# Performance work log

Hardware: AMD Instinct MI355X
Metric: run time of the kernel (lower is better)

## Reference

```python
import math
import jax, jax.numpy as jnp
import numpy as np

N, S, E, H = 8, 1024, 768, 12  # batch, seq_len, n_embed, n_head


def setup_inputs() -> dict:
    key = jax.random.key(0)
    ks = jax.random.split(key, 10)
    s = 1.0 / math.sqrt(E)
    x = jax.random.normal(ks[0], (N, S, E), dtype=jnp.float32)
    # per-head full-width projections, stacked over heads: [H, E, E] (Linear weight layout [out, in])
    Wq = jax.random.normal(ks[1], (H, E, E), dtype=jnp.float32) * s
    Wk = jax.random.normal(ks[2], (H, E, E), dtype=jnp.float32) * s
    Wv = jax.random.normal(ks[3], (H, E, E), dtype=jnp.float32) * s
    bq = jax.random.normal(ks[4], (H, E), dtype=jnp.float32) * s
    bk = jax.random.normal(ks[5], (H, E), dtype=jnp.float32) * s
    bv = jax.random.normal(ks[6], (H, E), dtype=jnp.float32) * s
    Wc = jax.random.normal(ks[7], (E, H * E), dtype=jnp.float32) * (1.0 / math.sqrt(H * E))
    bc = jax.random.normal(ks[8], (E,), dtype=jnp.float32) * s
    return {"x": x, "Wq": Wq, "bq": bq, "Wk": Wk, "bk": bk, "Wv": Wv, "bv": bv, "Wc": Wc, "bc": bc}


def reference(x, Wq, bq, Wk, bk, Wv, bv, Wc, bc):
    # Full-width QKV per head: [H, N, S, E]
    q = jnp.einsum('nse,hde->hnsd', x, Wq) + bq[:, None, None, :]
    k = jnp.einsum('nse,hde->hnsd', x, Wk) + bk[:, None, None, :]
    v = jnp.einsum('nse,hde->hnsd', x, Wv) + bv[:, None, None, :]
    # scores scaled by sqrt(n_embed) (source quirk: full n_embed, not head_dim)
    scores = jnp.einsum('hnsd,hntd->hnst', q, k) / math.sqrt(E)
    causal = jnp.tril(jnp.ones((S, S), dtype=bool))
    scores = jnp.where(causal[None, None, :, :], scores, -jnp.inf)
    # dropout applied before softmax in source; p=0 (eval) -> identity
    attn = jax.nn.softmax(scores, axis=-1)
    heads = jnp.einsum('hnst,hntd->hnsd', attn, v)  # [H, N, S, E]
    concat = jnp.transpose(heads, (1, 2, 0, 3)).reshape(N, S, H * E)
    return concat @ Wc.T + bc
```

## Files before the change

kernel.cpp:

```cpp
#include <hip/hip_runtime.h>
#include <hip/hip_bf16.h>
#include <stdint.h>

#define SEQ    1024
#define NBAT   8
#define EMB    768
#define NHEAD  12
#define MROWS  (NBAT*SEQ)
#define SCALE_S 0.03608439182435161f

typedef unsigned short u16;
typedef __attribute__((ext_vector_type(8))) short bf16x8;
typedef __attribute__((ext_vector_type(4))) float f32x4;

typedef void __attribute__((address_space(1)))* gas_ptr;
typedef void __attribute__((address_space(3)))* las_ptr;

__device__ __forceinline__ void gload16(const void* g, void* l) {
  __builtin_amdgcn_global_load_lds((gas_ptr)(void*)g, (las_ptr)l, 16, 0, 0);
}

#define VMCNT0 asm volatile("s_waitcnt vmcnt(0)" ::: "memory")
#define VMCNT2 asm volatile("s_waitcnt vmcnt(2)" ::: "memory")
#define VMCNT4 asm volatile("s_waitcnt vmcnt(4)" ::: "memory")
#define LGKM0  asm volatile("s_waitcnt lgkmcnt(0)" ::: "memory")
#define BARRIER asm volatile("s_barrier" ::: "memory")

__device__ __forceinline__ u16 f2bf(float f) {
  union { float f; uint32_t u; } a; a.f = f;
  uint32_t r = a.u + 0x7fffu + ((a.u >> 16) & 1u);
  return (u16)(r >> 16);
}
__device__ __forceinline__ uint32_t pack2(float a, float b) {
  return (uint32_t)f2bf(a) | ((uint32_t)f2bf(b) << 16);
}

__global__ void k_cvt(const float* __restrict__ s, u16* __restrict__ d, long n) {
  long i = ((long)blockIdx.x*blockDim.x + threadIdx.x)*8;
  if (i >= n) return;
  float4 a = *(const float4*)(s+i);
  float4 b = *(const float4*)(s+i+4);
  uint4 o; o.x = pack2(a.x,a.y); o.y = pack2(a.z,a.w);
  o.z = pack2(b.x,b.y); o.w = pack2(b.z,b.w);
  *(uint4*)(d+i) = o;
}

__global__ void k_cvt3(const float* __restrict__ s0, const float* __restrict__ s1,
                       const float* __restrict__ s2, u16* __restrict__ d0,
                       u16* __restrict__ d1, u16* __restrict__ d2, long n) {
  const float* s = blockIdx.z == 0 ? s0 : (blockIdx.z == 1 ? s1 : s2);
  u16* d = blockIdx.z == 0 ? d0 : (blockIdx.z == 1 ? d1 : d2);
  long i = ((long)blockIdx.x*blockDim.x + threadIdx.x)*8;
  if (i >= n) return;
  float4 a = *(const float4*)(s+i);
  float4 b = *(const float4*)(s+i+4);
  uint4 o; o.x = pack2(a.x,a.y); o.y = pack2(a.z,a.w);
  o.z = pack2(b.x,b.y); o.w = pack2(b.z,b.w);
  *(uint4*)(d+i) = o;
}

__global__ void k_cvtwc(const float* __restrict__ wc, u16* __restrict__ d, int Gi, int h0) {
  long ncol = (long)Gi*EMB;
  long i = ((long)blockIdx.x*blockDim.x + threadIdx.x)*4;
  if (i >= 768*ncol) return;
  long eo = i / ncol, c = i - eo*ncol;
  long g = c / EMB, dd = c - g*EMB;
  const float* s = wc + eo*(long)(NHEAD*EMB) + (h0+g)*EMB + dd;
  float4 a = *(const float4*)s;
  uint2 o; o.x = pack2(a.x,a.y); o.y = pack2(a.z,a.w);
  *(uint2*)(d+i) = o;
}

__global__ __launch_bounds__(512, 2) void k_gemm256(
    const u16* __restrict__ A, int lda,
    const u16* __restrict__ B, int ldb, int K,
    u16* __restrict__ Cb, long c_hs, int ldc,
    const float* __restrict__ bias, const float* __restrict__ bias2,
    int gsplit, int mode)
{
  __shared__ u16 lsA[2*16384];
  __shared__ u16 lsB[2*16384];

  int m0 = blockIdx.x * 256;
  int n0 = blockIdx.y * 256;
  int tid = threadIdx.x;
  int w = tid >> 6, l = tid & 63;
  int wr = w >> 2, wc = w & 3;

  const u16* gA = A + (size_t)(m0 + 32*w + (l>>3))*lda + (((l&7) ^ (l>>3)) << 3);
  const u16* gB = B + (size_t)(n0 + 32*w + (l>>3))*ldb + (((l&7) ^ (l>>3)) << 3);

#define STAGE256(t, buf) do { \
    int k0_ = (t)*64; \
    _Pragma("unroll") \
    for (int c_ = 0; c_ < 4; ++c_) \
      gload16(gA + (size_t)(c_*8)*lda + k0_, lsA + (buf)*16384 + (32*w + 8*c_)*64); \
    _Pragma("unroll") \
    for (int c_ = 0; c_ < 4; ++c_) \
      gload16(gB + (size_t)(c_*8)*ldb + k0_, lsB + (buf)*16384 + (32*w + 8*c_)*64); \
  } while(0)

  f32x4 acc[8][4];
  #pragma unroll
  for (int i = 0; i < 8; ++i)
    #pragma unroll
    for (int j = 0; j < 4; ++j) acc[i][j] = (f32x4)0.0f;

  int nt = K >> 6;
  STAGE256(0, 0);
  for (int t = 0; t < nt; ++t) {
    VMCNT0; BARRIER;
    if (t + 1 < nt) STAGE256(t+1, (t+1)&1);
    const u16* la = lsA + (t&1)*16384;
    const u16* lb = lsB + (t&1)*16384;
    #pragma unroll
    for (int ks = 0; ks < 2; ++ks) {
      int off = (((4*ks + (l>>4)) ^ (l&7)) << 3);
      bf16x8 af[8], bf_[4];
      #pragma unroll
      for (int fi = 0; fi < 8; ++fi)
        af[fi] = *(const bf16x8*)(la + (wr*128 + fi*16 + (l&15))*64 + off);
      #pragma unroll
      for (int fj = 0; fj < 4; ++fj)
        bf_[fj] = *(const bf16x8*)(lb + (wc*64 + fj*16 + (l&15))*64 + off);
      __builtin_amdgcn_s_setprio(1);
      #pragma unroll
      for (int fi = 0; fi < 8; ++fi)
        #pragma unroll
        for (int fj = 0; fj < 4; ++fj)
          acc[fi][fj] = __builtin_amdgcn_mfma_f32_16x16x32_bf16(af[fi], bf_[fj], acc[fi][fj], 0, 0, 0);
      __builtin_amdgcn_s_setprio(0);
    }
  }
#undef STAGE256

  if (mode == 0) {
    int s = n0 / 768;
    int dbase = n0 - s*768 + wc*64;
    const float* bsl = (s < gsplit) ? bias + (size_t)s*768 : bias2 + (size_t)(s - gsplit)*768;
    u16* Cs = Cb + (size_t)s*c_hs;
    #pragma unroll
    for (int fj = 0; fj < 4; ++fj) {
      int dcol = dbase + fj*16 + (l&15);
      float bb = bsl[dcol];
      #pragma unroll
      for (int fi = 0; fi < 8; ++fi) {
        #pragma unroll
        for (int r = 0; r < 4; ++r) {
          int row = m0 + wr*128 + fi*16 + (l>>4)*4 + r;
          Cs[(size_t)row*768 + dcol] = f2bf(acc[fi][fj][r] + bb);
        }
      }
    }
  } else {
    #pragma unroll
    for (int fi = 0; fi < 8; ++fi) {
      #pragma unroll
      for (int r = 0; r < 4; ++r) {
        int row = m0 + wr*128 + fi*16 + (l>>4)*4 + r;
        float bb = bias[row];
        #pragma unroll
        for (int fj = 0; fj < 4; ++fj) {
          int cbn = n0 + wc*64 + fj*16 + (l&15);
          Cb[(size_t)row*ldc + cbn] = f2bf(acc[fi][fj][r] + bb);
        }
      }
    }
  }
}

__global__ __launch_bounds__(256) void k_gemm(
    const u16* __restrict__ A, long a_hs, int lda,
    const u16* __restrict__ B, long b_hs, int ldb, int K,
    u16* Cb, float* Cf, long c_hs, int ldc,
    const float* __restrict__ bias, const float* __restrict__ bias2,
    long bias_hs, int gsplit, int mode, int swapxy)
{
  __shared__ u16 lsA[3*4096];
  __shared__ u16 lsB[3*4096];
  int g = blockIdx.z;
  const u16* Ag = A + (long)g*a_hs;
  const u16* Bg = B + (long)g*b_hs;
  int tm = swapxy ? blockIdx.y : blockIdx.x;
  int tn = swapxy ? blockIdx.x : blockIdx.y;
  int m0 = tm*128, n0 = tn*128;
  int tid = threadIdx.x;
  int w = tid >> 6, l = tid & 63;

  int srow = l >> 2;
  int scol = ((l & 3) ^ ((l >> 3) & 3)) * 8;
  const u16* ga0 = Ag + (long)(m0 + (2*w)*16   + srow)*lda + scol;
  const u16* ga1 = Ag + (long)(m0 + (2*w+1)*16 + srow)*lda + scol;
  const u16* gb0 = Bg + (long)(n0 + (2*w)*16   + srow)*ldb + scol;
  const u16* gb1 = Bg + (long)(n0 + (2*w+1)*16 + srow)*ldb + scol;

#define GSTAGE(k0, buf) do { \
// ... 48 lines not shown
#undef GSTAGE

  u16* Cbg = Cb ? Cb + (long)g*c_hs : (u16*)0;
  const float* bsel = (g < gsplit) ? bias : bias2;
  long gi = (g < gsplit) ? g : g - gsplit;
  const float* bs = bsel ? bsel + gi*bias_hs : (const float*)0;
  int rl = (l >> 4)*4, cl = l & 15;
  #pragma unroll
  for (int i = 0; i < 4; ++i) {
    #pragma unroll
    for (int j = 0; j < 4; ++j) {
      int rb = m0 + wr*64 + i*16 + rl;
      int cb = n0 + wc_*64 + j*16 + cl;
      float cbv = 0.f;
      if ((mode == 0 || mode == 2) && bs) cbv = bs[cb];
      #pragma unroll
      for (int r = 0; r < 4; ++r) {
        int rr = rb + r;
        float v = acc[i][j][r];
        v += (mode == 1) ? bs[rr] : cbv;
        size_t idx = (size_t)rr*(size_t)ldc + cb;
        if (mode <= 1) Cbg[idx] = f2bf(v);
        else if (mode == 2) Cf[idx] = v;
        else Cf[idx] += v;
      }
    }
  }
}

__global__ __launch_bounds__(512, 2) void k_attn(
    const u16* __restrict__ qb, const u16* __restrict__ kb,
    const u16* __restrict__ vtb, u16* __restrict__ hb, int ldh)
{
  __shared__ u16 kls[3*8192];
  __shared__ u16 vls[3*8192];
  __shared__ float s_t[64*68];
  __shared__ u16 p_t[64*64];
  __shared__ float e_s[64];

  int b = blockIdx.x;
  int xcd = b & 7, kk_ = b >> 3;
  int gn = xcd + 8*(kk_ >> 3), pair = kk_ & 7;
  int g = gn >> 3, n = gn & 7;

  const u16* Q  = qb  + (size_t)g*MROWS*EMB + (size_t)n*SEQ*EMB;
  const u16* Kp = kb  + (size_t)g*MROWS*EMB + (size_t)n*SEQ*EMB;
  const u16* Vt = vtb + (size_t)g*EMB*MROWS + (size_t)n*SEQ;
  u16* H = hb + (size_t)(n*SEQ)*ldh + (size_t)g*EMB;

  int tid = threadIdx.x;
  int w = tid >> 6, l = tid & 63;
  int qg = w >> 1;
  int cg = w & 1;
  int frow = l & 15;
  int fsw = frow & 7;
  int srow = tid >> 3;
  int sphys = tid & 7;
  int scol = ((sphys ^ (srow & 7)) << 3);

#define KSTAGE(base, pc, buf) do { \
    gload16((base) + (pc)*128,      kls + (buf)*8192 + w*512); \
    gload16((base) + (pc)*128 + 64, kls + (buf)*8192 + 4096 + w*512); \
  } while(0)
#define VSTAGE(vc, buf) do { \
    gload16(Vs + (size_t)((vc)*128)*MROWS,      vls + (buf)*8192 + w*512); \
    gload16(Vs + (size_t)((vc)*128 + 64)*MROWS, vls + (buf)*8192 + 4096 + w*512); \
  } while(0)

  for (int half = 0; half < 2; ++half) {
    int qt = half ? 15 - pair : pair;
    int q0 = qt * 64;
    int nt = qt + 1;

    f32x4 acc[6][4];
    #pragma unroll
    for (int i = 0; i < 6; ++i)
      #pragma unroll
      for (int j = 0; j < 4; ++j) acc[i][j] = (f32x4)0.0f;
    float m_reg = -1e30f, l_reg = 0.f;

    const u16* Qs = Q + (size_t)(q0 + srow)*EMB + scol;
    bf16x8 qreg[12][2];
    KSTAGE(Qs, 0, 0);
    KSTAGE(Qs, 1, 1);
    VMCNT2; BARRIER;
    #pragma unroll
    for (int pc = 0; pc < 6; ++pc) {
      if (pc < 4) KSTAGE(Qs, pc+2, (pc+2)%3);
      const u16* qb_ = kls + (pc%3)*8192;
      #pragma unroll
      for (int kk2 = 0; kk2 < 2; ++kk2)
        #pragma unroll
        for (int kkl = 0; kkl < 2; ++kkl)
          qreg[2*pc + kk2][kkl] = *(const bf16x8*)(qb_ + kk2*4096 + (qg*16 + frow)*64
                                                   + (((kkl*4 + (l>>4)) ^ fsw) << 3));
      if (pc < 4) { VMCNT2; } else if (pc == 4) { VMCNT0; }
      LGKM0; BARRIER;
    }

    for (int tt = 0; tt < nt; ++tt) {
      int t0 = tt*64;
      const u16* Ks = Kp + (size_t)(t0 + srow)*EMB + scol;
      const u16* Vs = Vt + (size_t)srow*MROWS + t0 + scol;
      if (tt == 0) { KSTAGE(Ks, 0, 0); KSTAGE(Ks, 1, 1); }
      VMCNT2; BARRIER;

      f32x4 sacc[2]; sacc[0] = (f32x4)0.0f; sacc[1] = (f32x4)0.0f;
      #pragma unroll
      for (int c = 0; c < 6; ++c) {
        if (c < 4)       KSTAGE(Ks, c+2, (c+2)%3);
        else if (c == 4) VSTAGE(0, 0);
        else             VSTAGE(1, 1);
        const u16* kb_ = kls + (c%3)*8192;
        __builtin_amdgcn_s_setprio(1);
        #pragma unroll
        for (int kk2 = 0; kk2 < 2; ++kk2) {
          #pragma unroll
          for (int kkl = 0; kkl < 2; ++kkl) {
            int so = ((kkl*4 + (l>>4)) ^ fsw) << 3;
            bf16x8 aq = qreg[2*c + kk2][kkl];
            #pragma unroll
            for (int cc = 0; cc < 2; ++cc) {
              bf16x8 bk_ = *(const bf16x8*)(kb_ + kk2*4096 + ((cg*2 + cc)*16 + frow)*64 + so);
              sacc[cc] = __builtin_amdgcn_mfma_f32_16x16x32_bf16(aq, bk_, sacc[cc], 0, 0, 0);
            }
          }
        }
        __builtin_amdgcn_s_setprio(0);
        if (c < 5) { VMCNT2; LGKM0; BARRIER; }
      }

      #pragma unroll
      for (int cc = 0; cc < 2; ++cc)
        #pragma unroll
        for (int r = 0; r < 4; ++r)
          s_t[(qg*16 + (l>>4)*4 + r)*68 + cg*32 + cc*16 + (l&15)] = sacc[cc][r]*SCALE_S;
      LGKM0; BARRIER;
      {
        int qglob = q0 + srow;
        int cbase = t0 + sphys*8;
        float v[8]; float mx = -1e30f;
        #pragma unroll
        for (int j = 0; j < 8; ++j) {
          float s = s_t[srow*68 + sphys*8 + j];
          if (cbase + j > qglob) s = -1e30f;
          v[j] = s; mx = fmaxf(mx, s);
        }
        mx = fmaxf(mx, __shfl_xor(mx, 1));
        mx = fmaxf(mx, __shfl_xor(mx, 2));
        mx = fmaxf(mx, __shfl_xor(mx, 4));
        float mn = fmaxf(m_reg, mx);
        float esc = __expf(m_reg - mn);
        float ps = 0.f; u16 pk[8];
        #pragma unroll
        for (int j = 0; j < 8; ++j) { float p = __expf(v[j] - mn); ps += p; pk[j] = f2bf(p); }
        ps += __shfl_xor(ps, 1); ps += __shfl_xor(ps, 2); ps += __shfl_xor(ps, 4);
        l_reg = l_reg*esc + ps; m_reg = mn;
        if (sphys == 0) e_s[srow] = esc;
        uint4 pv;
        pv.x = (uint32_t)pk[0] | ((uint32_t)pk[1] << 16);
        pv.y = (uint32_t)pk[2] | ((uint32_t)pk[3] << 16);
        pv.z = (uint32_t)pk[4] | ((uint32_t)pk[5] << 16);
        pv.w = (uint32_t)pk[6] | ((uint32_t)pk[7] << 16);
        *(uint4*)(p_t + srow*64 + ((sphys ^ (srow & 7)) << 3)) = pv;
      }
      VMCNT2; LGKM0; BARRIER;
      float er[4];
      #pragma unroll
      for (int r = 0; r < 4; ++r) er[r] = e_s[qg*16 + (l>>4)*4 + r];
      #pragma unroll
      for (int i = 0; i < 6; ++i)
        #pragma unroll
        for (int j = 0; j < 4; ++j)
          #pragma unroll
          for (int r = 0; r < 4; ++r) acc[i][j][r] *= er[r];
      bf16x8 pa[2];
      #pragma unroll
      for (int kk = 0; kk < 2; ++kk)
        pa[kk] = *(const bf16x8*)(p_t + (qg*16 + frow)*64 + (((kk*4 + (l>>4)) ^ fsw) << 3));
      bool stage_next = (tt + 1 < nt);
      const u16* Ks2 = Kp + (size_t)(t0 + 64 + srow)*EMB + scol;
      #pragma unroll
      for (int c = 0; c < 6; ++c) {
        if (c < 4)            VSTAGE(c+2, (c+2)%3);
        else if (stage_next)  { if (c == 4) KSTAGE(Ks2, 0, 0); else KSTAGE(Ks2, 1, 1); }
        const u16* vb_ = vls + (c%3)*8192;
        __builtin_amdgcn_s_setprio(1);
        #pragma unroll
        for (int cf = 0; cf < 4; ++cf) {
          #pragma unroll
          for (int kk = 0; kk < 2; ++kk) {
            bf16x8 vbf = *(const bf16x8*)(vb_ + (cg*64 + cf*16 + frow)*64 + (((kk*4 + (l>>4)) ^ fsw) << 3));
            acc[c][cf] = __builtin_amdgcn_mfma_f32_16x16x32_bf16(pa[kk], vbf, acc[c][cf], 0, 0, 0);
          }
        }
        __builtin_amdgcn_s_setprio(0);
        if (c < 4)      { VMCNT2; LGKM0; BARRIER; }
        else if (c == 4){ if (stage_next) { VMCNT2; } else { VMCNT0; } LGKM0; BARRIER; }
      }
    }
    if (sphys == 0) e_s[srow] = l_reg;
    LGKM0; BARRIER;
    float linv[4];
    #pragma unroll
    for (int r = 0; r < 4; ++r) linv[r] = 1.0f / e_s[qg*16 + (l>>4)*4 + r];
    #pragma unroll
    for (int i = 0; i < 6; ++i)
      #pragma unroll
      for (int j = 0; j < 4; ++j) {
        int col = i*128 + cg*64 + j*16 + (l & 15);
        #pragma unroll
        for (int r = 0; r < 4; ++r) {
          int row = q0 + qg*16 + (l>>4)*4 + r;
          H[(size_t)row*ldh + col] = f2bf(acc[i][j][r]*linv[r]);
        }
      }
    BARRIER;
  }
#undef KSTAGE
#undef VSTAGE
}

extern "C" void kernel_launch(void* const* d_in, const int* in_sizes, int n_in,
                              void* d_out, int out_size, void* d_ws, size_t ws_size,
                              hipStream_t stream) {
  const float* x  = (const float*)d_in[0];
  const float* Wq = (const float*)d_in[1];
  const float* bq = (const float*)d_in[2];
  const float* Wk = (const float*)d_in[3];
  const float* bk = (const float*)d_in[4];
  const float* Wv = (const float*)d_in[5];
  const float* bv = (const float*)d_in[6];
  const float* Wc = (const float*)d_in[7];
  const float* bc = (const float*)d_in[8];
  float* out = (float*)d_out;

  const size_t XB  = (size_t)MROWS*EMB*sizeof(u16);
  const size_t WHB = (size_t)EMB*EMB*sizeof(u16);
  const size_t per_g = 4*WHB + 4*XB;
  long long avail = (long long)ws_size - (long long)XB - 4096;
  int G = (int)(avail / (long long)per_g);
  if (G < 1) G = 1;
  if (G > NHEAD) G = NHEAD;

  char* ws = (char*)d_ws;
  u16* xb  = (u16*)ws;  ws += XB;
  u16* wqb = (u16*)ws;  ws += (size_t)(2*G)*WHB;
  u16* wvb = (u16*)ws;  ws += (size_t)G*WHB;
  u16* wcb = (u16*)ws;  ws += (size_t)G*WHB;
  u16* qb  = (u16*)ws;  ws += (size_t)(2*G)*XB;
  u16* vtb = (u16*)ws;  ws += (size_t)G*XB;
  u16* hbf = (u16*)ws;  ws += (size_t)G*XB;

  k_cvt<<<dim3(3072), dim3(256), 0, stream>>>(x, xb, (long)MROWS*EMB);

  for (int h0 = 0; h0 < NHEAD; h0 += G) {
    int Gi = (G < NHEAD - h0) ? G : (NHEAD - h0);
    long nw = (long)Gi*EMB*EMB;
    k_cvt3<<<dim3((unsigned)(nw/8/256), 1, 3), dim3(256), 0, stream>>>(
        Wq + (size_t)h0*EMB*EMB, Wk + (size_t)h0*EMB*EMB, Wv + (size_t)h0*EMB*EMB,
        wqb, wqb + (size_t)Gi*EMB*EMB, wvb, nw);
    k_cvtwc<<<dim3((unsigned)((768L*Gi*EMB/4)/256)), dim3(256), 0, stream>>>(Wc, wcb, Gi, h0);
    k_gemm256<<<dim3(32, 6*Gi), dim3(512), 0, stream>>>(
        xb, EMB, wqb, EMB, EMB,
        qb, (long)MROWS*EMB, 768,
        bq + (size_t)h0*EMB, bk + (size_t)h0*EMB, Gi, 0);
    k_gemm256<<<dim3(3*Gi, 32), dim3(512), 0, stream>>>(
        wvb, EMB, xb, EMB, EMB,
        vtb, 0L, MROWS,
        bv + (size_t)h0*EMB, (const float*)0, 9999, 1);
    k_attn<<<dim3(8*NBAT*Gi), dim3(512), 0, stream>>>(
        qb, qb + (size_t)Gi*MROWS*EMB, vtb, hbf, Gi*EMB);
    k_gemm<<<dim3(64, 6, 1), dim3(256), 0, stream>>>(
        hbf, 0L, Gi*EMB, wcb, 0L, Gi*EMB, Gi*EMB,
        (u16*)0, out, 0L, EMB,
        (h0 == 0 ? bc : (const float*)0), (const float*)0, 0L, 9999,
        (h0 == 0 ? 2 : 3), 0);
  }
}
```

Baseline: 1.144 ms.

## Restructure attention kernel with transposed MFMA tiles, register softmax, larger stages

Rewrites the attention kernel so scores are computed as K·Q^T with each wave owning a 32-key by 16-query slice. Softmax now runs directly on MFMA accumulator registers, using cross-wave max/sum exchange through small shared arrays instead of a full score tile in LDS. K/V staging moves to a unified 3-buffer pool with 256-wide chunks, fewer stage steps and barriers per tile, and a wider XOR swizzle. The output is written as packed 4-element bf16 stores. This adds more register pressure (24 Q fragments, 8 P fragments) and relies on new vmcnt accounting that could be fragile.

```diff
diff --git a/kernel.cpp b/kernel.cpp
--- a/kernel.cpp
+++ b/kernel.cpp
@@ -23,6 +23,7 @@
 #define VMCNT0 asm volatile("s_waitcnt vmcnt(0)" ::: "memory")
 #define VMCNT2 asm volatile("s_waitcnt vmcnt(2)" ::: "memory")
 #define VMCNT4 asm volatile("s_waitcnt vmcnt(4)" ::: "memory")
+#define VMCNT8 asm volatile("s_waitcnt vmcnt(8)" ::: "memory")
 #define LGKM0  asm volatile("s_waitcnt lgkmcnt(0)" ::: "memory")
 #define BARRIER asm volatile("s_barrier" ::: "memory")
 
@@ -276,11 +277,12 @@
     const u16* __restrict__ qb, const u16* __restrict__ kb,
     const u16* __restrict__ vtb, u16* __restrict__ hb, int ldh)
 {
-  __shared__ u16 kls[3*8192];
-  __shared__ u16 vls[3*8192];
-  __shared__ float s_t[64*68];
+  __shared__ u16 pool[3*16384];
   __shared__ u16 p_t[64*64];
-  __shared__ float e_s[64];
+  __shared__ float st_mx[128];
+  __shared__ float st_sm[128];
+  __shared__ float e_sc[64];
+  __shared__ float e_li[64];
 
   int b = blockIdx.x;
   int xcd = b & 7, kk_ = b >> 3;
@@ -294,27 +296,57 @@
 
   int tid = threadIdx.x;
   int w = tid >> 6, l = tid & 63;
-  int qg = w >> 1;
-  int cg = w & 1;
-  int frow = l & 15;
-  int fsw = frow & 7;
-  int srow = tid >> 3;
-  int sphys = tid & 7;
-  int scol = ((sphys ^ (srow & 7)) << 3);
-
-#define KSTAGE(base, pc, buf) do { \
-    gload16((base) + (pc)*128,      kls + (buf)*8192 + w*512); \
-    gload16((base) + (pc)*128 + 64, kls + (buf)*8192 + 4096 + w*512); \
+  int lo = l & 15, hi = l >> 4;
+  int khalf = w >> 2;
+  int qbase = (w & 3) * 16;
+  int myq = qbase + lo;
+  int kv0 = khalf*32 + lo;
+  int kv1 = kv0 + 16;
+
+#define KSTAGE(base, ch, buf) do { \
+    _Pragma("unroll") for (int i_ = 0; i_ < 4; ++i_) { \
+      int u_ = tid + 512*i_; \
+      gload16((base) + (size_t)(u_>>5)*EMB + ((ch)*256 + (((u_&31) ^ ((u_>>5)&31))<<3)), \
+              pool + (buf)*16384 + ((w*64 + 512*i_)<<3)); \
+    } } while(0)
+#define VSTAGE(t0v, ch, buf) do { \
+    _Pragma("unroll") for (int i_ = 0; i_ < 4; ++i_) { \
+      int u_ = tid + 512*i_; \
+      gload16(Vt + (size_t)((ch)*256 + (u_>>3))*MROWS + (t0v) + (((u_&7) ^ ((u_>>3)&7))<<3), \
+              pool + (buf)*16384 + ((w*64 + 512*i_)<<3)); \
+    } } while(0)
+
+#define QK_COMPUTE(ch) do { \
+    const u16* kb_ = pool + (ch)*16384; \
+    __builtin_amdgcn_s_setprio(1); \
+    _Pragma("unroll") for (int ks = 0; ks < 8; ++ks) { \
+      bf16x8 k0_ = *(const bf16x8*)(kb_ + ((kv0*32 + ((ks*4 + hi) ^ (kv0 & 31)))<<3)); \
+      bf16x8 k1_ = *(const bf16x8*)(kb_ + ((kv1*32 + ((ks*4 + hi) ^ (kv1 & 31)))<<3)); \
+      sacc0 = __builtin_amdgcn_mfma_f32_16x16x32_bf16(k0_, qreg[(ch)*8+ks], sacc0, 0, 0, 0); \
+      sacc1 = __builtin_amdgcn_mfma_f32_16x16x32_bf16(k1_, qreg[(ch)*8+ks], sacc1, 0, 0, 0); \
+    } \
+    __builtin_amdgcn_s_setprio(0); \
   } while(0)
-#define VSTAGE(vc, buf) do { \
-    gload16(Vs + (size_t)((vc)*128)*MROWS,      vls + (buf)*8192 + w*512); \
-    gload16(Vs + (size_t)((vc)*128 + 64)*MROWS, vls + (buf)*8192 + 4096 + w*512); \
+
+#define PV_COMPUTE(ch) do { \
+    const u16* vb_ = pool + (ch)*16384; \
+    __builtin_amdgcn_s_setprio(1); \
+    _Pragma("unroll") for (int jp = 0; jp < 2; ++jp) { \
+      int el_ = (w + 8*jp)*16 + lo; \
+      _Pragma("unroll") for (int ks2 = 0; ks2 < 2; ++ks2) { \
+        bf16x8 vf_ = *(const bf16x8*)(vb_ + (((el_<<3) + ((ks2*4 + hi) ^ (el_ & 7)))<<3)); \
+        _Pragma("unroll") for (int qf = 0; qf < 4; ++qf) \
+          acc[2*(ch)+jp][qf] = __builtin_amdgcn_mfma_f32_16x16x32_bf16(vf_, pf[ks2][qf], acc[2*(ch)+jp][qf], 0, 0, 0); \
+      } \
+    } \
+    __builtin_amdgcn_s_setprio(0); \
   } while(0)
 
   for (int half = 0; half < 2; ++half) {
     int qt = half ? 15 - pair : pair;
     int q0 = qt * 64;
     int nt = qt + 1;
+    int qabs = q0 + myq;
 
     f32x4 acc[6][4];
     #pragma unroll
@@ -323,146 +355,135 @@
       for (int j = 0; j < 4; ++j) acc[i][j] = (f32x4)0.0f;
     float m_reg = -1e30f, l_reg = 0.f;
 
-    const u16* Qs = Q + (size_t)(q0 + srow)*EMB + scol;
-    bf16x8 qreg[12][2];
-    KSTAGE(Qs, 0, 0);
-    KSTAGE(Qs, 1, 1);
-    VMCNT2; BARRIER;
-    #pragma unroll
-    for (int pc = 0; pc < 6; ++pc) {
-      if (pc < 4) KSTAGE(Qs, pc+2, (pc+2)%3);
-      const u16* qb_ = kls + (pc%3)*8192;
-      #pragma unroll
-      for (int kk2 = 0; kk2 < 2; ++kk2)
-        #pragma unroll
-        for (int kkl = 0; kkl < 2; ++kkl)
-          qreg[2*pc + kk2][kkl] = *(const bf16x8*)(qb_ + kk2*4096 + (qg*16 + frow)*64
-                                                   + (((kkl*4 + (l>>4)) ^ fsw) << 3));
-      if (pc < 4) { VMCNT2; } else if (pc == 4) { VMCNT0; }
-      LGKM0; BARRIER;
-    }
+    const u16* Qb = Q + (size_t)q0*EMB;
+    VMCNT0;
+    KSTAGE(Qb, 0, 0);
+    KSTAGE(Qb, 1, 1);
+    KSTAGE(Qb, 2, 2);
+    VMCNT8; BARRIER;
+    bf16x8 qreg[24];
+    #pragma unroll
+    for (int ks = 0; ks < 8; ++ks)
+      qreg[ks] = *(const bf16x8*)(pool + ((myq*32 + ((ks*4 + hi) ^ (myq & 31)))<<3));
+    VMCNT4; LGKM0; BARRIER;
+    KSTAGE(Kp, 0, 0);
+    #pragma unroll
+    for (int ks = 0; ks < 8; ++ks)
+      qreg[8+ks] = *(const bf16x8*)(pool + 16384 + ((myq*32 + ((ks*4 + hi) ^ (myq & 31)))<<3));
+    VMCNT4; LGKM0; BARRIER;
+    KSTAGE(Kp, 1, 1);
+    #pragma unroll
+    for (int ks = 0; ks < 8; ++ks)
+      qreg[16+ks] = *(const bf16x8*)(pool + 2*16384 + ((myq*32 + ((ks*4 + hi) ^ (myq & 31)))<<3));
+    VMCNT4; LGKM0; BARRIER;
 
     for (int tt = 0; tt < nt; ++tt) {
       int t0 = tt*64;
-      const u16* Ks = Kp + (size_t)(t0 + srow)*EMB + scol;
-      const u16* Vs = Vt + (size_t)srow*MROWS + t0 + scol;
-      if (tt == 0) { KSTAGE(Ks, 0, 0); KSTAGE(Ks, 1, 1); }
-      VMCNT2; BARRIER;
-
-      f32x4 sacc[2]; sacc[0] = (f32x4)0.0f; sacc[1] = (f32x4)0.0f;
-      #pragma unroll
-      for (int c = 0; c < 6; ++c) {
-        if (c < 4)       KSTAGE(Ks, c+2, (c+2)%3);
-        else if (c == 4) VSTAGE(0, 0);
-        else             VSTAGE(1, 1);
-        const u16* kb_ = kls + (c%3)*8192;
-        __builtin_amdgcn_s_setprio(1);
+      int nt0 = (tt + 1 < nt) ? (tt+1)*64 : 0;
+      f32x4 sacc0 = (f32x4)0.0f, sacc1 = (f32x4)0.0f;
+
+      KSTAGE(Kp + (size_t)t0*EMB, 2, 2);
+      QK_COMPUTE(0);
+      VMCNT4; LGKM0; BARRIER;
+      VSTAGE(t0, 0, 0);
+      QK_COMPUTE(1);
+      VMCNT4; LGKM0; BARRIER;
+      VSTAGE(t0, 1, 1);
+      QK_COMPUTE(2);
+      VMCNT4; LGKM0; BARRIER;
+
+      VSTAGE(t0, 2, 2);
+      float pm = -1e30f;
+      {
+        int kvb = t0 + khalf*32 + hi*4;
         #pragma unroll
-        for (int kk2 = 0; kk2 < 2; ++kk2) {
-          #pragma unroll
-          for (int kkl = 0; kkl < 2; ++kkl) {
-            int so = ((kkl*4 + (l>>4)) ^ fsw) << 3;
-            bf16x8 aq = qreg[2*c + kk2][kkl];
-            #pragma unroll
-            for (int cc = 0; cc < 2; ++cc) {
-              bf16x8 bk_ = *(const bf16x8*)(kb_ + kk2*4096 + ((cg*2 + cc)*16 + frow)*64 + so);
-              sacc[cc] = __builtin_amdgcn_mfma_f32_16x16x32_bf16(aq, bk_, sacc[cc], 0, 0, 0);
-            }
-          }
+        for (int r = 0; r < 4; ++r) {
+          float x0 = sacc0[r]*SCALE_S;
+          float x1 = sacc1[r]*SCALE_S;
+          if (kvb + r > qabs)      x0 = -1e30f;
+          if (kvb + 16 + r > qabs) x1 = -1e30f;
+          sacc0[r] = x0; sacc1[r] = x1;
+          pm = fmaxf(pm, fmaxf(x0, x1));
         }
-        __builtin_amdgcn_s_setprio(0);
-        if (c < 5) { VMCNT2; LGKM0; BARRIER; }
       }
-
-      #pragma unroll
-      for (int cc = 0; cc < 2; ++cc)
+      pm = fmaxf(pm, __shfl_xor(pm, 16));
+      pm = fmaxf(pm, __shfl_xor(pm, 32));
+      if (l < 16) st_mx[khalf*64 + myq] = pm;
+      LGKM0; BARRIER;
+      float mn = fmaxf(m_reg, fmaxf(st_mx[myq], st_mx[64 + myq]));
+      float esc = __expf(m_reg - mn);
+      m_reg = mn;
+      float p0_ = __expf(sacc0[0]-mn), p1_ = __expf(sacc0[1]-mn);
+      float p2_ = __expf(sacc0[2]-mn), p3_ = __expf(sacc0[3]-mn);
+      float p4_ = __expf(sacc1[0]-mn), p5_ = __expf(sacc1[1]-mn);
+      float p6_ = __expf(sacc1[2]-mn), p7_ = __expf(sacc1[3]-mn);
+      float ps = ((p0_+p1_)+(p2_+p3_)) + ((p4_+p5_)+(p6_+p7_));
+      ps += __shfl_xor(ps, 16);
+      ps += __shfl_xor(ps, 32);
+      if (l < 16) { st_sm[khalf*64 + myq] = ps; if (khalf == 0) e_sc[myq] = esc; }
+      {
+        int sl0 = khalf*4 + (hi>>1);
+        int ph0 = sl0 ^ (myq & 7);
+        int ph1 = (sl0 + 2) ^ (myq & 7);
+        uint2 v0; v0.x = pack2(p0_, p1_); v0.y = pack2(p2_, p3_);
+        uint2 v1; v1.x = pack2(p4_, p5_); v1.y = pack2(p6_, p7_);
+        *(uint2*)(p_t + myq*64 + ph0*8 + (hi&1)*4) = v0;
+        *(uint2*)(p_t + myq*64 + ph1*8 + (hi&1)*4) = v1;
+      }
+      LGKM0; BARRIER;
+      l_reg = l_reg*esc + st_sm[myq] + st_sm[64 + myq];
+
+      bf16x8 pf[2][4];
+      #pragma unroll
+      for (int ks2 = 0; ks2 < 2; ++ks2)
         #pragma unroll
-        for (int r = 0; r < 4; ++r)
-          s_t[(qg*16 + (l>>4)*4 + r)*68 + cg*32 + cc*16 + (l&15)] = sacc[cc][r]*SCALE_S;
-      LGKM0; BARRIER;
-      {
-        int qglob = q0 + srow;
-        int cbase = t0 + sphys*8;
-        float v[8]; float mx = -1e30f;
-        #pragma unroll
-        for (int j = 0; j < 8; ++j) {
-          float s = s_t[srow*68 + sphys*8 + j];
-          if (cbase + j > qglob) s = -1e30f;
-          v[j] = s; mx = fmaxf(mx, s);
+        for (int qf = 0; qf < 4; ++qf) {
+          int qr = qf*16 + lo;
+          pf[ks2][qf] = *(const bf16x8*)(p_t + ((qr*8 + ((ks2*4 + hi) ^ (qr & 7)))<<3));
         }
-        mx = fmaxf(mx, __shfl_xor(mx, 1));
-        mx = fmaxf(mx, __shfl_xor(mx, 2));
-        mx = fmaxf(mx, __shfl_xor(mx, 4));
-        float mn = fmaxf(m_reg, mx);
-        float esc = __expf(m_reg - mn);
-        float ps = 0.f; u16 pk[8];
-        #pragma unroll
-        for (int j = 0; j < 8; ++j) { float p = __expf(v[j] - mn); ps += p; pk[j] = f2bf(p); }
-        ps += __shfl_xor(ps, 1); ps += __shfl_xor(ps, 2); ps += __shfl_xor(ps, 4);
-        l_reg = l_reg*esc + ps; m_reg = mn;
-        if (sphys == 0) e_s[srow] = esc;
-        uint4 pv;
-        pv.x = (uint32_t)pk[0] | ((uint32_t)pk[1] << 16);
-        pv.y = (uint32_t)pk[2] | ((uint32_t)pk[3] << 16);
-        pv.z = (uint32_t)pk[4] | ((uint32_t)pk[5] << 16);
-        pv.w = (uint32_t)pk[6] | ((uint32_t)pk[7] << 16);
-        *(uint4*)(p_t + srow*64 + ((sphys ^ (srow & 7)) << 3)) = pv;
-      }
-      VMCNT2; LGKM0; BARRIER;
-      float er[4];
-      #pragma unroll
-      for (int r = 0; r < 4; ++r) er[r] = e_s[qg*16 + (l>>4)*4 + r];
+      float escq[4];
+      #pragma unroll
+      for (int qf = 0; qf < 4; ++qf) escq[qf] = e_sc[qf*16 + lo];
       #pragma unroll
       for (int i = 0; i < 6; ++i)
         #pragma unroll
-        for (int j = 0; j < 4; ++j)
+        for (int qf = 0; qf < 4; ++qf)
           #pragma unroll
-          for (int r = 0; r < 4; ++r) acc[i][j][r] *= er[r];
-      bf16x8 pa[2];
-      #pragma unroll
-      for (int kk = 0; kk < 2; ++kk)
-        pa[kk] = *(const bf16x8*)(p_t + (qg*16 + frow)*64 + (((kk*4 + (l>>4)) ^ fsw) << 3));
-      bool stage_next = (tt + 1 < nt);
-      const u16* Ks2 = Kp + (size_t)(t0 + 64 + srow)*EMB + scol;
-      #pragma unroll
-      for (int c = 0; c < 6; ++c) {
-        if (c < 4)            VSTAGE(c+2, (c+2)%3);
-        else if (stage_next)  { if (c == 4) KSTAGE(Ks2, 0, 0); else KSTAGE(Ks2, 1, 1); }
-        const u16* vb_ = vls + (c%3)*8192;
-        __builtin_amdgcn_s_setprio(1);
-        #pragma unroll
-        for (int cf = 0; cf < 4; ++cf) {
-          #pragma unroll
-          for (int kk = 0; kk < 2; ++kk) {
-            bf16x8 vbf = *(const bf16x8*)(vb_ + (cg*64 + cf*16 + frow)*64 + (((kk*4 + (l>>4)) ^ fsw) << 3));
-            acc[c][cf] = __builtin_amdgcn_mfma_f32_16x16x32_bf16(pa[kk], vbf, acc[c][cf], 0, 0, 0);
-          }
-        }
-        __builtin_amdgcn_s_setprio(0);
-        if (c < 4)      { VMCNT2; LGKM0; BARRIER; }
-        else if (c == 4){ if (stage_next) { VMCNT2; } else { VMCNT0; } LGKM0; BARRIER; }
+          for (int r = 0; r < 4; ++r) acc[i][qf][r] *= escq[qf];
+
+      PV_COMPUTE(0);
+      VMCNT4; LGKM0; BARRIER;
+      KSTAGE(Kp + (size_t)nt0*EMB, 0, 0);
+      PV_COMPUTE(1);
+      VMCNT4; LGKM0; BARRIER;
+      KSTAGE(Kp + (size_t)nt0*EMB, 1, 1);
+      PV_COMPUTE(2);
+      VMCNT4; LGKM0; BARRIER;
+    }
+
+    if (l < 16 && khalf == 0) e_li[myq] = 1.0f / l_reg;
+    LGKM0; BARRIER;
+    float li[4];
+    #pragma unroll
+    for (int qf = 0; qf < 4; ++qf) li[qf] = e_li[qf*16 + lo];
+    #pragma unroll
+    for (int j = 0; j < 6; ++j) {
+      int e_g = (j>>1)*256 + (w + 8*(j&1))*16 + hi*4;
+      #pragma unroll
+      for (int qf = 0; qf < 4; ++qf) {
+        int q_abs2 = q0 + qf*16 + lo;
+        uint2 v;
+        v.x = pack2(acc[j][qf][0]*li[qf], acc[j][qf][1]*li[qf]);
+        v.y = pack2(acc[j][qf][2]*li[qf], acc[j][qf][3]*li[qf]);
+        *(uint2*)(H + (size_t)q_abs2*ldh + e_g) = v;
       }
     }
-    if (sphys == 0) e_s[srow] = l_reg;
-    LGKM0; BARRIER;
-    float linv[4];
-    #pragma unroll
-    for (int r = 0; r < 4; ++r) linv[r] = 1.0f / e_s[qg*16 + (l>>4)*4 + r];
-    #pragma unroll
-    for (int i = 0; i < 6; ++i)
-      #pragma unroll
-      for (int j = 0; j < 4; ++j) {
-        int col = i*128 + cg*64 + j*16 + (l & 15);
-        #pragma unroll
-        for (int r = 0; r < 4; ++r) {
-          int row = q0 + qg*16 + (l>>4)*4 + r;
-          H[(size_t)row*ldh + col] = f2bf(acc[i][j][r]*linv[r]);
-        }
-      }
     BARRIER;
   }
 #undef KSTAGE
 #undef VSTAGE
+#undef QK_COMPUTE
+#undef PV_COMPUTE
 }
 
 extern "C" void kernel_launch(void* const* d_in, const int* in_sizes, int n_in,
```

Result: slower. 2.112 ms (+84.5%).

## Shrink QKV GEMM tile to 256x128 and add triple-buffered LDS prefetch

Applied to the files above, without the earlier changes.

The 256-wide GEMM now computes 256x128 output tiles, with 8 waves laid out 4x2 and each wave holding a 64x64 accumulator. LDS goes from double to triple buffering with two stages prefetched ahead, and the wait becomes a partial vmcnt(6) so the next tile's loads can stay in flight during compute. Smaller accumulators cut register pressure and double the number of blocks launched, at the cost of more redundant loads of A per output and lower MFMA reuse per LDS read.

```diff
diff --git a/kernel.cpp b/kernel.cpp
--- a/kernel.cpp
+++ b/kernel.cpp
@@ -23,6 +23,7 @@
 #define VMCNT0 asm volatile("s_waitcnt vmcnt(0)" ::: "memory")
 #define VMCNT2 asm volatile("s_waitcnt vmcnt(2)" ::: "memory")
 #define VMCNT4 asm volatile("s_waitcnt vmcnt(4)" ::: "memory")
+#define VMCNT6 asm volatile("s_waitcnt vmcnt(6)" ::: "memory")
 #define LGKM0  asm volatile("s_waitcnt lgkmcnt(0)" ::: "memory")
 #define BARRIER asm volatile("s_barrier" ::: "memory")
 
@@ -78,17 +79,18 @@
     const float* __restrict__ bias, const float* __restrict__ bias2,
     int gsplit, int mode)
 {
-  __shared__ u16 lsA[2*16384];
-  __shared__ u16 lsB[2*16384];
+  __shared__ u16 lsA[3*16384];
+  __shared__ u16 lsB[3*8192];
 
   int m0 = blockIdx.x * 256;
-  int n0 = blockIdx.y * 256;
+  int n0 = blockIdx.y * 128;
   int tid = threadIdx.x;
   int w = tid >> 6, l = tid & 63;
-  int wr = w >> 2, wc = w & 3;
+  int wr = w >> 1, wc = w & 1;
+  int lo = l & 15, hi = l >> 4;
 
   const u16* gA = A + (size_t)(m0 + 32*w + (l>>3))*lda + (((l&7) ^ (l>>3)) << 3);
-  const u16* gB = B + (size_t)(n0 + 32*w + (l>>3))*ldb + (((l&7) ^ (l>>3)) << 3);
+  const u16* gB = B + (size_t)(n0 + 16*w + (l>>3))*ldb + (((l&7) ^ (l>>3)) << 3);
 
 #define STAGE256(t, buf) do { \
     int k0_ = (t)*64; \
@@ -96,36 +98,45 @@
     for (int c_ = 0; c_ < 4; ++c_) \
       gload16(gA + (size_t)(c_*8)*lda + k0_, lsA + (buf)*16384 + (32*w + 8*c_)*64); \
     _Pragma("unroll") \
-    for (int c_ = 0; c_ < 4; ++c_) \
-      gload16(gB + (size_t)(c_*8)*ldb + k0_, lsB + (buf)*16384 + (32*w + 8*c_)*64); \
+    for (int c_ = 0; c_ < 2; ++c_) \
+      gload16(gB + (size_t)(c_*8)*ldb + k0_, lsB + (buf)*8192 + (16*w + 8*c_)*64); \
   } while(0)
 
-  f32x4 acc[8][4];
+  f32x4 acc[4][4];
   #pragma unroll
-  for (int i = 0; i < 8; ++i)
+  for (int i = 0; i < 4; ++i)
     #pragma unroll
     for (int j = 0; j < 4; ++j) acc[i][j] = (f32x4)0.0f;
 
   int nt = K >> 6;
   STAGE256(0, 0);
+  STAGE256(1, 1);
   for (int t = 0; t < nt; ++t) {
-    VMCNT0; BARRIER;
-    if (t + 1 < nt) STAGE256(t+1, (t+1)&1);
-    const u16* la = lsA + (t&1)*16384;
-    const u16* lb = lsB + (t&1)*16384;
+    if (t + 1 < nt) { VMCNT6; } else { VMCNT0; }
+    BARRIER;
+    if (t + 2 < nt) {
+      int nb = t + 2; nb -= (nb/3)*3;
+      STAGE256(t+2, nb);
+    }
+    int cb = t - (t/3)*3;
+    const u16* la = lsA + cb*16384;
+    const u16* lb = lsB + cb*8192;
     #pragma unroll
     for (int ks = 0; ks < 2; ++ks) {
-      int off = (((4*ks + (l>>4)) ^ (l&7)) << 3);
-      bf16x8 af[8], bf_[4];
-      #pragma unroll
-      for (int fi = 0; fi < 8; ++fi)
-        af[fi] = *(const bf16x8*)(la + (wr*128 + fi*16 + (l&15))*64 + off);
-      #pragma unroll
-      for (int fj = 0; fj < 4; ++fj)
-        bf_[fj] = *(const bf16x8*)(lb + (wc*64 + fj*16 + (l&15))*64 + off);
+      bf16x8 af[4], bf_[4];
+      #pragma unroll
+      for (int fi = 0; fi < 4; ++fi) {
+        int row = wr*64 + fi*16 + lo;
+        af[fi] = *(const bf16x8*)(la + row*64 + (((4*ks + hi) ^ (row & 7)) << 3));
+      }
+      #pragma unroll
+      for (int fj = 0; fj < 4; ++fj) {
+        int row = wc*64 + fj*16 + lo;
+        bf_[fj] = *(const bf16x8*)(lb + row*64 + (((4*ks + hi) ^ (row & 7)) << 3));
+      }
       __builtin_amdgcn_s_setprio(1);
       #pragma unroll
-      for (int fi = 0; fi < 8; ++fi)
+      for (int fi = 0; fi < 4; ++fi)
         #pragma unroll
         for (int fj = 0; fj < 4; ++fj)
           acc[fi][fj] = __builtin_amdgcn_mfma_f32_16x16x32_bf16(af[fi], bf_[fj], acc[fi][fj], 0, 0, 0);
@@ -141,27 +152,27 @@
     u16* Cs = Cb + (size_t)s*c_hs;
     #pragma unroll
     for (int fj = 0; fj < 4; ++fj) {
-      int dcol = dbase + fj*16 + (l&15);
+      int dcol = dbase + fj*16 + lo;
       float bb = bsl[dcol];
       #pragma unroll
-      for (int fi = 0; fi < 8; ++fi) {
+      for (int fi = 0; fi < 4; ++fi) {
         #pragma unroll
         for (int r = 0; r < 4; ++r) {
-          int row = m0 + wr*128 + fi*16 + (l>>4)*4 + r;
+          int row = m0 + wr*64 + fi*16 + hi*4 + r;
           Cs[(size_t)row*768 + dcol] = f2bf(acc[fi][fj][r] + bb);
         }
       }
     }
   } else {
     #pragma unroll
-    for (int fi = 0; fi < 8; ++fi) {
+    for (int fi = 0; fi < 4; ++fi) {
       #pragma unroll
       for (int r = 0; r < 4; ++r) {
-        int row = m0 + wr*128 + fi*16 + (l>>4)*4 + r;
+        int row = m0 + wr*64 + fi*16 + hi*4 + r;
         float bb = bias[row];
         #pragma unroll
         for (int fj = 0; fj < 4; ++fj) {
-          int cbn = n0 + wc*64 + fj*16 + (l&15);
+          int cbn = n0 + wc*64 + fj*16 + lo;
           Cb[(size_t)row*ldc + cbn] = f2bf(acc[fi][fj][r] + bb);
         }
       }
@@ -505,11 +516,11 @@
         Wq + (size_t)h0*EMB*EMB, Wk + (size_t)h0*EMB*EMB, Wv + (size_t)h0*EMB*EMB,
         wqb, wqb + (size_t)Gi*EMB*EMB, wvb, nw);
     k_cvtwc<<<dim3((unsigned)((768L*Gi*EMB/4)/256)), dim3(256), 0, stream>>>(Wc, wcb, Gi, h0);
-    k_gemm256<<<dim3(32, 6*Gi), dim3(512), 0, stream>>>(
+    k_gemm256<<<dim3(32, 12*Gi), dim3(512), 0, stream>>>(
         xb, EMB, wqb, EMB, EMB,
         qb, (long)MROWS*EMB, 768,
         bq + (size_t)h0*EMB, bk + (size_t)h0*EMB, Gi, 0);
-    k_gemm256<<<dim3(3*Gi, 32), dim3(512), 0, stream>>>(
+    k_gemm256<<<dim3(3*Gi, 64), dim3(512), 0, stream>>>(
         wvb, EMB, xb, EMB, EMB,
         vtb, 0L, MROWS,
         bv + (size_t)h0*EMB, (const float*)0, 9999, 1);
```

Measured after the change: 1.198 ms. 4.7% more time.

## Widen attention KV tile to 128 keys with a shared triple-buffered LDS pool

Applied to the files above, without the earlier changes.

The attention kernel now processes 128 keys per iteration instead of 64, halving the number of softmax/rescale/barrier rounds and doubling the MFMA work per staged chunk. K, V and Q staging share one triple-buffered LDS pool with four 16-byte loads per thread per chunk, and the wait counts are adjusted to match. The 128-key tile means half the tiles on the diagonal are partly masked, so some wasted compute is added for causal blocks. LDS use per block also rises, which may hurt the two-blocks-per-CU occupancy.

```diff
diff --git a/kernel.cpp b/kernel.cpp
--- a/kernel.cpp
+++ b/kernel.cpp
@@ -23,6 +23,7 @@
 #define VMCNT0 asm volatile("s_waitcnt vmcnt(0)" ::: "memory")
 #define VMCNT2 asm volatile("s_waitcnt vmcnt(2)" ::: "memory")
 #define VMCNT4 asm volatile("s_waitcnt vmcnt(4)" ::: "memory")
+#define VMCNT8 asm volatile("s_waitcnt vmcnt(8)" ::: "memory")
 #define LGKM0  asm volatile("s_waitcnt lgkmcnt(0)" ::: "memory")
 #define BARRIER asm volatile("s_barrier" ::: "memory")
 
@@ -276,10 +277,9 @@
     const u16* __restrict__ qb, const u16* __restrict__ kb,
     const u16* __restrict__ vtb, u16* __restrict__ hb, int ldh)
 {
-  __shared__ u16 kls[3*8192];
-  __shared__ u16 vls[3*8192];
-  __shared__ float s_t[64*68];
-  __shared__ u16 p_t[64*64];
+  __shared__ u16 pool[3*16384];
+  __shared__ float s_t[64*132];
+  __shared__ u16 p_t[64*128];
   __shared__ float e_s[64];
 
   int b = blockIdx.x;
@@ -296,25 +296,68 @@
   int w = tid >> 6, l = tid & 63;
   int qg = w >> 1;
   int cg = w & 1;
-  int frow = l & 15;
-  int fsw = frow & 7;
+  int lo = l & 15, hi = l >> 4;
+  int fsw = lo & 7;
   int srow = tid >> 3;
   int sphys = tid & 7;
   int scol = ((sphys ^ (srow & 7)) << 3);
 
-#define KSTAGE(base, pc, buf) do { \
-    gload16((base) + (pc)*128,      kls + (buf)*8192 + w*512); \
-    gload16((base) + (pc)*128 + 64, kls + (buf)*8192 + 4096 + w*512); \
-  } while(0)
-#define VSTAGE(vc, buf) do { \
-    gload16(Vs + (size_t)((vc)*128)*MROWS,      vls + (buf)*8192 + w*512); \
-    gload16(Vs + (size_t)((vc)*128 + 64)*MROWS, vls + (buf)*8192 + 4096 + w*512); \
+#define KSTAGE128(kbase, ch, buf) do { \
+    gload16((kbase) + (size_t)(srow)*EMB      + (ch)*128 +      scol, pool + (buf)*16384 + w*512); \
+    gload16((kbase) + (size_t)(srow + 64)*EMB + (ch)*128 +      scol, pool + (buf)*16384 + w*512 + 4096); \
+    gload16((kbase) + (size_t)(srow)*EMB      + (ch)*128 + 64 + scol, pool + (buf)*16384 + w*512 + 8192); \
+    gload16((kbase) + (size_t)(srow + 64)*EMB + (ch)*128 + 64 + scol, pool + (buf)*16384 + w*512 + 12288); \
+  } while(0)
+#define VSTAGE128(ch, buf, t0v) do { \
+    gload16(Vt + (size_t)((ch)*128 + srow)*MROWS      + (t0v) +      scol, pool + (buf)*16384 + w*512); \
+    gload16(Vt + (size_t)((ch)*128 + srow + 64)*MROWS + (t0v) +      scol, pool + (buf)*16384 + w*512 + 4096); \
+    gload16(Vt + (size_t)((ch)*128 + srow)*MROWS      + (t0v) + 64 + scol, pool + (buf)*16384 + w*512 + 8192); \
+    gload16(Vt + (size_t)((ch)*128 + srow + 64)*MROWS + (t0v) + 64 + scol, pool + (buf)*16384 + w*512 + 12288); \
+  } while(0)
+#define QSTAGE(pc, buf) do { \
+    const u16* qs_ = Q + (size_t)(q0 + srow)*EMB + (pc)*128 + scol; \
+    gload16(qs_,      pool + (buf)*16384 + w*512); \
+    gload16(qs_ + 64, pool + (buf)*16384 + w*512 + 4096); \
+  } while(0)
+#define QREAD(pc, buf) do { \
+    _Pragma("unroll") for (int kk2 = 0; kk2 < 2; ++kk2) \
+      _Pragma("unroll") for (int kkl = 0; kkl < 2; ++kkl) \
+        qreg[(pc)*4 + kk2*2 + kkl] = *(const bf16x8*)(pool + (buf)*16384 + kk2*4096 \
+             + (qg*16 + lo)*64 + (((kkl*4 + hi) ^ fsw) << 3)); \
+  } while(0)
+#define QK_PHASE(ch, buf) do { \
+    const u16* kb_ = pool + (buf)*16384; \
+    __builtin_amdgcn_s_setprio(1); \
+    _Pragma("unroll") for (int kk2 = 0; kk2 < 2; ++kk2) \
+      _Pragma("unroll") for (int kkl = 0; kkl < 2; ++kkl) { \
+        bf16x8 aq = qreg[(ch)*4 + kk2*2 + kkl]; \
+        int so = ((kkl*4 + hi) ^ fsw) << 3; \
+        _Pragma("unroll") for (int cc = 0; cc < 4; ++cc) { \
+          bf16x8 bk_ = *(const bf16x8*)(kb_ + kk2*8192 + ((cg*4 + cc)*16 + lo)*64 + so); \
+          sacc[cc] = __builtin_amdgcn_mfma_f32_16x16x32_bf16(aq, bk_, sacc[cc], 0, 0, 0); \
+        } \
+      } \
+    __builtin_amdgcn_s_setprio(0); \
+  } while(0)
+#define PV_PHASE(ch, buf) do { \
+    const u16* vb_ = pool + (buf)*16384; \
+    __builtin_amdgcn_s_setprio(1); \
+    _Pragma("unroll") for (int kk = 0; kk < 4; ++kk) { \
+      int so = (((kk&1)*4 + hi) ^ fsw) << 3; \
+      const u16* ph_ = vb_ + (kk>>1)*8192; \
+      _Pragma("unroll") for (int cf = 0; cf < 4; ++cf) { \
+        bf16x8 vf_ = *(const bf16x8*)(ph_ + (cg*64 + cf*16 + lo)*64 + so); \
+        acc[(ch)][cf] = __builtin_amdgcn_mfma_f32_16x16x32_bf16(pa[kk], vf_, acc[(ch)][cf], 0, 0, 0); \
+      } \
+    } \
+    __builtin_amdgcn_s_setprio(0); \
   } while(0)
 
   for (int half = 0; half < 2; ++half) {
     int qt = half ? 15 - pair : pair;
     int q0 = qt * 64;
-    int nt = qt + 1;
+    int ntk = (qt >> 1) + 1;
+    int qglob = q0 + srow;
 
     f32x4 acc[6][4];
     #pragma unroll
@@ -323,71 +366,49 @@
       for (int j = 0; j < 4; ++j) acc[i][j] = (f32x4)0.0f;
     float m_reg = -1e30f, l_reg = 0.f;
 
-    const u16* Qs = Q + (size_t)(q0 + srow)*EMB + scol;
-    bf16x8 qreg[12][2];
-    KSTAGE(Qs, 0, 0);
-    KSTAGE(Qs, 1, 1);
+    bf16x8 qreg[24];
+    VMCNT0;
+    QSTAGE(0, 0); QSTAGE(1, 1);
     VMCNT2; BARRIER;
-    #pragma unroll
-    for (int pc = 0; pc < 6; ++pc) {
-      if (pc < 4) KSTAGE(Qs, pc+2, (pc+2)%3);
-      const u16* qb_ = kls + (pc%3)*8192;
-      #pragma unroll
-      for (int kk2 = 0; kk2 < 2; ++kk2)
-        #pragma unroll
-        for (int kkl = 0; kkl < 2; ++kkl)
-          qreg[2*pc + kk2][kkl] = *(const bf16x8*)(qb_ + kk2*4096 + (qg*16 + frow)*64
-                                                   + (((kkl*4 + (l>>4)) ^ fsw) << 3));
-      if (pc < 4) { VMCNT2; } else if (pc == 4) { VMCNT0; }
+    QSTAGE(2, 2);        QREAD(0, 0); VMCNT2; LGKM0; BARRIER;
+    QSTAGE(3, 0);        QREAD(1, 1); VMCNT2; LGKM0; BARRIER;
+    QSTAGE(4, 1);        QREAD(2, 2); VMCNT2; LGKM0; BARRIER;
+    QSTAGE(5, 2);        QREAD(3, 0); VMCNT2; LGKM0; BARRIER;
+    KSTAGE128(Kp, 0, 0); QREAD(4, 1); VMCNT4; LGKM0; BARRIER;
+    KSTAGE128(Kp, 1, 1); QREAD(5, 2);
+
+    for (int tt = 0; tt < ntk; ++tt) {
+      int t0 = tt*128;
+      const u16* Kb  = Kp + (size_t)t0*EMB;
+      const u16* Kbn = Kp + (size_t)(t0 + 128)*EMB;
+      bool sn = (tt + 1 < ntk);
+
+      VMCNT4; BARRIER;
+      f32x4 sacc[4];
+      #pragma unroll
+      for (int cc = 0; cc < 4; ++cc) sacc[cc] = (f32x4)0.0f;
+
+      KSTAGE128(Kb, 2, 2);  QK_PHASE(0, 0);  VMCNT4; LGKM0; BARRIER;
+      KSTAGE128(Kb, 3, 0);  QK_PHASE(1, 1);  VMCNT4; LGKM0; BARRIER;
+      KSTAGE128(Kb, 4, 1);  QK_PHASE(2, 2);  VMCNT4; LGKM0; BARRIER;
+      KSTAGE128(Kb, 5, 2);  QK_PHASE(3, 0);  VMCNT4; LGKM0; BARRIER;
+      VSTAGE128(0, 0, t0);  QK_PHASE(4, 1);  VMCNT4; LGKM0; BARRIER;
+      VSTAGE128(1, 1, t0);  QK_PHASE(5, 2);
+      #pragma unroll
+      for (int cc = 0; cc < 4; ++cc)
+        #pragma unroll
+        for (int r = 0; r < 4; ++r)
+          s_t[(qg*16 + hi*4 + r)*132 + (cg*4 + cc)*16 + lo] = sacc[cc][r]*SCALE_S;
       LGKM0; BARRIER;
-    }
-
-    for (int tt = 0; tt < nt; ++tt) {
-      int t0 = tt*64;
-      const u16* Ks = Kp + (size_t)(t0 + srow)*EMB + scol;
-      const u16* Vs = Vt + (size_t)srow*MROWS + t0 + scol;
-      if (tt == 0) { KSTAGE(Ks, 0, 0); KSTAGE(Ks, 1, 1); }
-      VMCNT2; BARRIER;
-
-      f32x4 sacc[2]; sacc[0] = (f32x4)0.0f; sacc[1] = (f32x4)0.0f;
-      #pragma unroll
-      for (int c = 0; c < 6; ++c) {
-        if (c < 4)       KSTAGE(Ks, c+2, (c+2)%3);
-        else if (c == 4) VSTAGE(0, 0);
-        else             VSTAGE(1, 1);
-        const u16* kb_ = kls + (c%3)*8192;
-        __builtin_amdgcn_s_setprio(1);
-        #pragma unroll
-        for (int kk2 = 0; kk2 < 2; ++kk2) {
-          #pragma unroll
-          for (int kkl = 0; kkl < 2; ++kkl) {
-            int so = ((kkl*4 + (l>>4)) ^ fsw) << 3;
-            bf16x8 aq = qreg[2*c + kk2][kkl];
-            #pragma unroll
-            for (int cc = 0; cc < 2; ++cc) {
-              bf16x8 bk_ = *(const bf16x8*)(kb_ + kk2*4096 + ((cg*2 + cc)*16 + frow)*64 + so);
-              sacc[cc] = __builtin_amdgcn_mfma_f32_16x16x32_bf16(aq, bk_, sacc[cc], 0, 0, 0);
-            }
-          }
-        }
-        __builtin_amdgcn_s_setprio(0);
-        if (c < 5) { VMCNT2; LGKM0; BARRIER; }
-      }
-
-      #pragma unroll
-      for (int cc = 0; cc < 2; ++cc)
-        #pragma unroll
-        for (int r = 0; r < 4; ++r)
-          s_t[(qg*16 + (l>>4)*4 + r)*68 + cg*32 + cc*16 + (l&15)] = sacc[cc][r]*SCALE_S;
-      LGKM0; BARRIER;
+
+      VSTAGE128(2, 2, t0);
       {
-        int qglob = q0 + srow;
-        int cbase = t0 + sphys*8;
-        float v[8]; float mx = -1e30f;
-        #pragma unroll
-        for (int j = 0; j < 8; ++j) {
-          float s = s_t[srow*68 + sphys*8 + j];
-          if (cbase + j > qglob) s = -1e30f;
+        int cb0 = t0 + sphys*16;
+        float v[16]; float mx = -1e30f;
+        #pragma unroll
+        for (int j = 0; j < 16; ++j) {
+          float s = s_t[srow*132 + sphys*16 + j];
+          if (cb0 + j > qglob) s = -1e30f;
           v[j] = s; mx = fmaxf(mx, s);
         }
         mx = fmaxf(mx, __shfl_xor(mx, 1));
@@ -395,74 +416,76 @@
         mx = fmaxf(mx, __shfl_xor(mx, 4));
         float mn = fmaxf(m_reg, mx);
         float esc = __expf(m_reg - mn);
-        float ps = 0.f; u16 pk[8];
-        #pragma unroll
-        for (int j = 0; j < 8; ++j) { float p = __expf(v[j] - mn); ps += p; pk[j] = f2bf(p); }
+        float ps = 0.f; u16 pk[16];
+        #pragma unroll
+        for (int j = 0; j < 16; ++j) { float p = __expf(v[j] - mn); ps += p; pk[j] = f2bf(p); }
         ps += __shfl_xor(ps, 1); ps += __shfl_xor(ps, 2); ps += __shfl_xor(ps, 4);
         l_reg = l_reg*esc + ps; m_reg = mn;
         if (sphys == 0) e_s[srow] = esc;
-        uint4 pv;
-        pv.x = (uint32_t)pk[0] | ((uint32_t)pk[1] << 16);
-        pv.y = (uint32_t)pk[2] | ((uint32_t)pk[3] << 16);
-        pv.z = (uint32_t)pk[4] | ((uint32_t)pk[5] << 16);
-        pv.w = (uint32_t)pk[6] | ((uint32_t)pk[7] << 16);
-        *(uint4*)(p_t + srow*64 + ((sphys ^ (srow & 7)) << 3)) = pv;
+        uint4 w0, w1;
+        w0.x = (uint32_t)pk[0]  | ((uint32_t)pk[1]  << 16);
+        w0.y = (uint32_t)pk[2]  | ((uint32_t)pk[3]  << 16);
+        w0.z = (uint32_t)pk[4]  | ((uint32_t)pk[5]  << 16);
+        w0.w = (uint32_t)pk[6]  | ((uint32_t)pk[7]  << 16);
+        w1.x = (uint32_t)pk[8]  | ((uint32_t)pk[9]  << 16);
+        w1.y = (uint32_t)pk[10] | ((uint32_t)pk[11] << 16);
+        w1.z = (uint32_t)pk[12] | ((uint32_t)pk[13] << 16);
+        w1.w = (uint32_t)pk[14] | ((uint32_t)pk[15] << 16);
+        *(uint4*)(p_t + srow*128 + (((2*sphys)     ^ (srow & 7)) << 3)) = w0;
+        *(uint4*)(p_t + srow*128 + (((2*sphys + 1) ^ (srow & 7)) << 3)) = w1;
       }
-      VMCNT2; LGKM0; BARRIER;
+      VMCNT8; LGKM0; BARRIER;
+
       float er[4];
       #pragma unroll
-      for (int r = 0; r < 4; ++r) er[r] = e_s[qg*16 + (l>>4)*4 + r];
+      for (int r = 0; r < 4; ++r) er[r] = e_s[qg*16 + hi*4 + r];
       #pragma unroll
       for (int i = 0; i < 6; ++i)
         #pragma unroll
         for (int j = 0; j < 4; ++j)
           #pragma unroll
           for (int r = 0; r < 4; ++r) acc[i][j][r] *= er[r];
-      bf16x8 pa[2];
-      #pragma unroll
-      for (int kk = 0; kk < 2; ++kk)
-        pa[kk] = *(const bf16x8*)(p_t + (qg*16 + frow)*64 + (((kk*4 + (l>>4)) ^ fsw) << 3));
-      bool stage_next = (tt + 1 < nt);
-      const u16* Ks2 = Kp + (size_t)(t0 + 64 + srow)*EMB + scol;
-      #pragma unroll
-      for (int c = 0; c < 6; ++c) {
-        if (c < 4)            VSTAGE(c+2, (c+2)%3);
-        else if (stage_next)  { if (c == 4) KSTAGE(Ks2, 0, 0); else KSTAGE(Ks2, 1, 1); }
-        const u16* vb_ = vls + (c%3)*8192;
-        __builtin_amdgcn_s_setprio(1);
-        #pragma unroll
-        for (int cf = 0; cf < 4; ++cf) {
-          #pragma unroll
-          for (int kk = 0; kk < 2; ++kk) {
-            bf16x8 vbf = *(const bf16x8*)(vb_ + (cg*64 + cf*16 + frow)*64 + (((kk*4 + (l>>4)) ^ fsw) << 3));
-            acc[c][cf] = __builtin_amdgcn_mfma_f32_16x16x32_bf16(pa[kk], vbf, acc[c][cf], 0, 0, 0);
-          }
-        }
-        __builtin_amdgcn_s_setprio(0);
-        if (c < 4)      { VMCNT2; LGKM0; BARRIER; }
-        else if (c == 4){ if (stage_next) { VMCNT2; } else { VMCNT0; } LGKM0; BARRIER; }
-      }
+      bf16x8 pa[4];
+      #pragma unroll
+      for (int kk = 0; kk < 4; ++kk)
+        pa[kk] = *(const bf16x8*)(p_t + (qg*16 + lo)*128 + (((kk*4 + hi) ^ fsw) << 3));
+
+                             PV_PHASE(0, 0);  VMCNT4; LGKM0; BARRIER;
+      VSTAGE128(3, 0, t0);   PV_PHASE(1, 1);  VMCNT4; LGKM0; BARRIER;
+      VSTAGE128(4, 1, t0);   PV_PHASE(2, 2);  VMCNT4; LGKM0; BARRIER;
+      VSTAGE128(5, 2, t0);   PV_PHASE(3, 0);  VMCNT4; LGKM0; BARRIER;
+      if (sn) KSTAGE128(Kbn, 0, 0);
+                             PV_PHASE(4, 1);
+      if (sn) { VMCNT4; } else { VMCNT0; }
+      LGKM0; BARRIER;
+      if (sn) KSTAGE128(Kbn, 1, 1);
+                             PV_PHASE(5, 2);
     }
+
     if (sphys == 0) e_s[srow] = l_reg;
     LGKM0; BARRIER;
     float linv[4];
     #pragma unroll
-    for (int r = 0; r < 4; ++r) linv[r] = 1.0f / e_s[qg*16 + (l>>4)*4 + r];
+    for (int r = 0; r < 4; ++r) linv[r] = 1.0f / e_s[qg*16 + hi*4 + r];
     #pragma unroll
     for (int i = 0; i < 6; ++i)
       #pragma unroll
       for (int j = 0; j < 4; ++j) {
-        int col = i*128 + cg*64 + j*16 + (l & 15);
+        int col = i*128 + cg*64 + j*16 + lo;
         #pragma unroll
         for (int r = 0; r < 4; ++r) {
-          int row = q0 + qg*16 + (l>>4)*4 + r;
+          int row = q0 + qg*16 + hi*4 + r;
           H[(size_t)row*ldh + col] = f2bf(acc[i][j][r]*linv[r]);
         }
       }
     BARRIER;
   }
-#undef KSTAGE
-#undef VSTAGE
+#undef KSTAGE128
+#undef VSTAGE128
+#undef QSTAGE
+#undef QREAD
+#undef QK_PHASE
+#undef PV_PHASE
 }
 
 extern "C" void kernel_launch(void* const* d_in, const int* in_sizes, int n_in,
```

Measured after the change: 1.250 ms. +9.3%, slower.
